# Optimization experiments

Measured on AMD Instinct MI355X. Metric: run time of the kernel, lower is better.

The kernel has to match this reference:

```python
import jax, jax.numpy as jnp
import numpy as np

N_NODES = 50000
N_EDGES = 1600000
IN_DIM = 512
OUT_DIM = 256


def setup_inputs() -> dict:
    key = jax.random.key(0)
    k1, k2, k3, k4, k5, k6 = jax.random.split(key, 6)
    inputs = jax.random.normal(k1, (N_NODES, IN_DIM), dtype=jnp.float32)
    edge_row = jax.random.randint(k2, (N_EDGES,), 0, N_NODES, dtype=jnp.int32)
    edge_col = jax.random.randint(k3, (N_EDGES,), 0, N_NODES, dtype=jnp.int32)
    edge_val = jax.random.uniform(k4, (N_EDGES,), dtype=jnp.float32)
    stdv = 1.0 / np.sqrt(OUT_DIM)
    weight = jax.random.uniform(k5, (IN_DIM, OUT_DIM), dtype=jnp.float32, minval=-stdv, maxval=stdv)
    bias = jax.random.uniform(k6, (OUT_DIM,), dtype=jnp.float32, minval=-stdv, maxval=stdv)
    return {"inputs": inputs, "edge_row": edge_row, "edge_col": edge_col,
            "edge_val": edge_val, "weight": weight, "bias": bias}


def reference(inputs, edge_row, edge_col, edge_val, weight, bias):
    # dense GEMM: [N, in] @ [in, out] -> [N, out]
    support = inputs @ weight
    # SpMM: out[r] += val * support[c] for each edge (r, c, val)
    gathered = edge_val[:, None] * support[edge_col]  # [E, out]
    output = jax.ops.segment_sum(gathered, edge_row, num_segments=N_NODES)
    return output + bias
```

## Files before the change

kernel.cpp:

```cpp
#include <hip/hip_runtime.h>

#define N_NODES 50000
#define N_EDGES 1600000
#define IN_DIM 512
#define OUT_DIM 256

#define BM 128
#define BN 256
#define BK 32
#define APAD 8
#define LDA (BK + APAD)

#define RPB   128
#define NBKT  391
#define CHUNK 4096
#define CAP   5120

typedef unsigned int u32;
typedef unsigned short u16;
typedef short bf16x8 __attribute__((ext_vector_type(8)));
typedef float f32x4 __attribute__((ext_vector_type(4)));

__device__ __forceinline__ float bf_to_f(u16 u) { return __uint_as_float(((u32)u) << 16); }
__device__ __forceinline__ u16 f_to_bf(float f) {
    u32 u = __float_as_uint(f);
    u32 r = (u + 0x7fffu + ((u >> 16) & 1u)) >> 16;
    return (u16)r;
}

__global__ __launch_bounds__(256) void zero_cur(int* __restrict__ cursor) {
    const int i = blockIdx.x * 256 + threadIdx.x;
    if (i < NBKT) cursor[i] = 0;
}

__global__ __launch_bounds__(256) void scatter1(const int* __restrict__ er,
                                                const int* __restrict__ ec,
                                                const float* __restrict__ ev,
                                                int* __restrict__ cursor,
                                                int2* __restrict__ tmp) {
    __shared__ int  hcnt[NBKT];
    __shared__ int  loff[NBKT];
    __shared__ int  gbase[NBKT];
    __shared__ int  sc[512];
    __shared__ int2 estage[CHUNK];
    __shared__ u16  bslot[CHUNK];

    const int t = threadIdx.x;
    const int base = blockIdx.x * CHUNK;
    const int nedge = min(CHUNK, N_EDGES - base);

    for (int k = t; k < NBKT; k += 256) hcnt[k] = 0;
    __syncthreads();

    int w0[16], w1[16], rk[16];
    #pragma unroll
    for (int j = 0; j < 16; ++j) {
        const int i = j * 256 + t;
        rk[j] = -1;
        if (i < nedge) {
            const int e = base + i;
            const int r = er[e];
            const int bk = r >> 7;
            w0[j] = ec[e] | ((r & 127) << 16) | (bk << 23);
            w1[j] = __float_as_int(ev[e]);
            rk[j] = atomicAdd(&hcnt[bk], 1);
        }
    }
    __syncthreads();

    sc[t]       = (t < NBKT) ? hcnt[t] : 0;
    sc[t + 256] = (t + 256 < NBKT) ? hcnt[t + 256] : 0;
    __syncthreads();
    #pragma unroll
    for (int off = 1; off < 512; off <<= 1) {
        const int a0 = (t >= off) ? sc[t - off] : 0;
        const int a1 = sc[t + 256 - off];
        __syncthreads();
        sc[t] += a0;
        sc[t + 256] += a1;
        __syncthreads();
    }
    if (t < NBKT)       loff[t]       = sc[t] - hcnt[t];
    if (t + 256 < NBKT) loff[t + 256] = sc[t + 256] - hcnt[t + 256];

    if (t < NBKT && hcnt[t] > 0)
        gbase[t] = t * CAP + atomicAdd(&cursor[t], hcnt[t]);
    if (t + 256 < NBKT && hcnt[t + 256] > 0)
        gbase[t + 256] = (t + 256) * CAP + atomicAdd(&cursor[t + 256], hcnt[t + 256]);
    __syncthreads();

    #pragma unroll
    for (int j = 0; j < 16; ++j) {
        if (rk[j] >= 0) {
            const int bk = ((u32)w0[j]) >> 23;
            const int s = loff[bk] + rk[j];
            estage[s] = make_int2(w0[j], w1[j]);
            bslot[s]  = (u16)bk;
        }
    }
    __syncthreads();

    for (int s = t; s < nedge; s += 256) {
        const int bk = bslot[s];
        const int2 e2 = estage[s];
        const int gpos = gbase[bk] + (s - loff[bk]);
        if (gpos < (bk + 1) * CAP)
            tmp[gpos] = e2;
    }
}

__global__ __launch_bounds__(256) void bscan(const int* __restrict__ cursor,
                                             int* __restrict__ bucket_base,
                                             int* __restrict__ row_ptr) {
    __shared__ int sc[512];
    __shared__ int orig[512];
    const int t = threadIdx.x;
    const int c0 = (t < NBKT) ? min(cursor[t], CAP) : 0;
    const int c1 = (t + 256 < NBKT) ? min(cursor[t + 256], CAP) : 0;
    sc[t] = c0;       orig[t] = c0;
    sc[t + 256] = c1; orig[t + 256] = c1;
    __syncthreads();
    #pragma unroll
    for (int off = 1; off < 512; off <<= 1) {
        const int a0 = (t >= off) ? sc[t - off] : 0;
        const int a1 = sc[t + 256 - off];
        __syncthreads();
        sc[t] += a0;
        sc[t + 256] += a1;
        __syncthreads();
    }
    if (t < NBKT)       bucket_base[t]       = sc[t] - orig[t];
    if (t + 256 < NBKT) bucket_base[t + 256] = sc[t + 256] - orig[t + 256];
    if (t == 0) row_ptr[N_NODES] = N_EDGES;
}

__global__ __launch_bounds__(256) void scatter2(const int* __restrict__ cursor,
                                                const int* __restrict__ bucket_base,
                                                const int2* __restrict__ tmp,
                                                int* __restrict__ row_ptr,
                                                int2* __restrict__ sedge) {
    __shared__ int rcnt[RPB];
    __shared__ int sc[RPB];
    __shared__ int rcur[RPB];
    const int t = threadIdx.x;
    const int b = blockIdx.x;
    const int n = min(cursor[b], CAP);
    const int2* src = tmp + (size_t)b * CAP;
    const int gb = bucket_base[b];

    if (t < RPB) rcnt[t] = 0;
    __syncthreads();
    for (int i = t; i < n; i += 256)
        atomicAdd(&rcnt[(((u32)src[i].x) >> 16) & 127], 1);
    __syncthreads();

    if (t < RPB) sc[t] = rcnt[t];
    __syncthreads();
    #pragma unroll
    for (int off = 1; off < RPB; off <<= 1) {
        int a = 0;
        if (t < RPB && t >= off) a = sc[t - off];
        __syncthreads();
        if (t < RPB) sc[t] += a;
        __syncthreads();
    }
    if (t < RPB) {
        const int excl = sc[t] - rcnt[t];
        rcur[t] = gb + excl;
        const int row = b * RPB + t;
        if (row < N_NODES) row_ptr[row] = gb + excl;
    }
    __syncthreads();

    for (int i = t; i < n; i += 256) {
        const int2 e2 = src[i];
        const int rloc = (((u32)e2.x) >> 16) & 127;
        const int pos = atomicAdd(&rcur[rloc], 1);
        sedge[pos] = make_int2(e2.x & 0xFFFF, e2.y);
    }
}

__global__ __launch_bounds__(256) void wcvt(const float* __restrict__ W,
                                            u16* __restrict__ WT) {
    const int n  = threadIdx.x;
    const int k0 = blockIdx.x * 4;
    ushort4 o;
    o.x = f_to_bf(W[(size_t)(k0 + 0) * OUT_DIM + n]);
    o.y = f_to_bf(W[(size_t)(k0 + 1) * OUT_DIM + n]);
    o.z = f_to_bf(W[(size_t)(k0 + 2) * OUT_DIM + n]);
    o.w = f_to_bf(W[(size_t)(k0 + 3) * OUT_DIM + n]);
    *(ushort4*)(WT + (size_t)n * IN_DIM + k0) = o;
}

__global__ __launch_bounds__(512) void gemm_mfma(const float* __restrict__ X,
                                                 const u16* __restrict__ WT,
                                                 u16* __restrict__ Sb) {
    __shared__ u16 As[BM * LDA];
    __shared__ u16 Bs[BN * LDA];

    const int tid  = threadIdx.x;
    const int wave = tid >> 6;
    const int lane = tid & 63;
    const int r0   = blockIdx.x * BM;
    const int wm   = (wave & 1) * 64;
    const int wn   = (wave >> 1) * 64;
    const int l15  = lane & 15;
    const int quad = lane >> 4;

    f32x4 acc[4][4];
    #pragma unroll
    for (int i = 0; i < 4; ++i)
        #pragma unroll
        for (int j = 0; j < 4; ++j) acc[i][j] = (f32x4)0.f;

    const int arow = tid >> 2;
    const int akp  = (tid & 3) * 8;
    const int xrow = min(r0 + arow, N_NODES - 1);
    const float* xsrc = X + (size_t)xrow * IN_DIM + akp;
    const int brow = tid >> 1;
    const int bkp  = (tid & 1) * 16;
    const u16* bsrc = WT + (size_t)brow * IN_DIM + bkp;

    for (int kc = 0; kc < IN_DIM; kc += BK) {
        {
            const float4 f0 = *(const float4*)(xsrc + kc + 0);
            const float4 f1 = *(const float4*)(xsrc + kc + 4);
            ushort4 p0, p1;
            p0.x = f_to_bf(f0.x); p0.y = f_to_bf(f0.y); p0.z = f_to_bf(f0.z); p0.w = f_to_bf(f0.w);
            p1.x = f_to_bf(f1.x); p1.y = f_to_bf(f1.y); p1.z = f_to_bf(f1.z); p1.w = f_to_bf(f1.w);
            *(ushort4*)&As[arow * LDA + akp + 0] = p0;
            *(ushort4*)&As[arow * LDA + akp + 4] = p1;
        }
        {
            const uint4 b0 = *(const uint4*)(bsrc + kc);
            const uint4 b1 = *(const uint4*)(bsrc + kc + 8);
            *(uint4*)&Bs[brow * LDA + bkp + 0] = b0;
            *(uint4*)&Bs[brow * LDA + bkp + 8] = b1;
        }
        __syncthreads();

        bf16x8 af[4], bfr[4];
        #pragma unroll
        for (int mt = 0; mt < 4; ++mt)
            af[mt] = *(const bf16x8*)&As[(wm + mt * 16 + l15) * LDA + quad * 8];
        #pragma unroll
        for (int nt = 0; nt < 4; ++nt)
            bfr[nt] = *(const bf16x8*)&Bs[(wn + nt * 16 + l15) * LDA + quad * 8];
        #pragma unroll
        for (int mt = 0; mt < 4; ++mt)
            #pragma unroll
            for (int nt = 0; nt < 4; ++nt)
                acc[mt][nt] = __builtin_amdgcn_mfma_f32_16x16x32_bf16(
                    af[mt], bfr[nt], acc[mt][nt], 0, 0, 0);
        __syncthreads();
    }

    #pragma unroll
    for (int mt = 0; mt < 4; ++mt) {
        #pragma unroll
        for (int r = 0; r < 4; ++r) {
            const int grow = r0 + wm + mt * 16 + quad * 4 + r;
            if (grow < N_NODES) {
                u16* dst = Sb + (size_t)grow * OUT_DIM + wn + l15;
                #pragma unroll
                for (int nt = 0; nt < 4; ++nt)
                    dst[nt * 16] = f_to_bf(acc[mt][nt][r]);
            }
        }
    }
}

__global__ __launch_bounds__(256) void csr_spmm(const int* __restrict__ row_ptr,
                                                const int2* __restrict__ sedge,
                                                const u16* __restrict__ Sb,
                                                const float* __restrict__ bias,
                                                float* __restrict__ out) {
    const int wave = threadIdx.x >> 6;
    const int lane = threadIdx.x & 63;
    const int r = blockIdx.x * 4 + wave;
    if (r >= N_NODES) return;

    const int start = row_ptr[r];
    const int end   = row_ptr[r + 1];

    float4 acc = *(const float4*)(bias + lane * 4);
    const u16* sbase = Sb + lane * 4;
    const long long* se = (const long long*)sedge;

    for (int e = start; e < end; e += 8) {
        int   cols[8];
        float vals[8];
        #pragma unroll
        for (int j = 0; j < 8; ++j) {
            const int idx = min(e + j, end - 1);
            const long long ed = __builtin_nontemporal_load(se + idx);
            cols[j] = (int)(u32)ed;
            vals[j] = (e + j < end) ? __int_as_float((int)(ed >> 32)) : 0.f;
        }

        ushort4 sv[8];
        #pragma unroll
        for (int j = 0; j < 8; ++j)
            sv[j] = *(const ushort4*)(sbase + (size_t)cols[j] * OUT_DIM);

        #pragma unroll
        for (int j = 0; j < 8; ++j) {
            acc.x += vals[j] * bf_to_f(sv[j].x);
            acc.y += vals[j] * bf_to_f(sv[j].y);
            acc.z += vals[j] * bf_to_f(sv[j].z);
            acc.w += vals[j] * bf_to_f(sv[j].w);
        }
    }

    float* dst = out + (size_t)r * OUT_DIM + lane * 4;
    __builtin_nontemporal_store(acc.x, dst + 0);
    __builtin_nontemporal_store(acc.y, dst + 1);
    __builtin_nontemporal_store(acc.z, dst + 2);
    __builtin_nontemporal_store(acc.w, dst + 3);
}

extern "C" void kernel_launch(void* const* d_in, const int* in_sizes, int n_in,
                              void* d_out, int out_size, void* d_ws, size_t ws_size,
                              hipStream_t stream) {
    const float* X    = (const float*)d_in[0];
    const int*   er   = (const int*)d_in[1];
    const int*   ec   = (const int*)d_in[2];
    const float* ev   = (const float*)d_in[3];
    const float* W    = (const float*)d_in[4];
    const float* bias = (const float*)d_in[5];
    float* out        = (float*)d_out;

    char* ws = (char*)d_ws;
    u16*  Sb      = (u16*) (ws);
    int2* tmp     = (int2*)(ws);
    int*  cursor  = (int*) (ws + 16100000);
    int*  bbase   = (int*) (ws + 16110000);
    int2* sedge   = (int2*)(ws + 25600000);
    u16*  WT      = (u16*) (ws + 38400000);
    int*  row_ptr = (int*) (ws + 38662144);

    hipLaunchKernelGGL(zero_cur, dim3(2), dim3(256), 0, stream, cursor);
    hipLaunchKernelGGL(scatter1, dim3((N_EDGES + CHUNK - 1) / CHUNK), dim3(256), 0,
                       stream, er, ec, ev, cursor, tmp);
    hipLaunchKernelGGL(bscan, dim3(1), dim3(256), 0, stream, cursor, bbase, row_ptr);
    hipLaunchKernelGGL(scatter2, dim3(NBKT), dim3(256), 0, stream,
                       cursor, bbase, tmp, row_ptr, sedge);
    hipLaunchKernelGGL(wcvt, dim3(IN_DIM / 4), dim3(256), 0, stream, W, WT);
    hipLaunchKernelGGL(gemm_mfma, dim3((N_NODES + BM - 1) / BM), dim3(512), 0,
                       stream, X, WT, Sb);
    hipLaunchKernelGGL(csr_spmm, dim3((N_NODES + 3) / 4), dim3(256), 0, stream,
                       row_ptr, sedge, Sb, bias, out);
}
```

Before: 376.3 us.

## Fold bucket scan into scatter2, shrink GEMM tile, simplify SpMM edge loads

```diff
diff --git a/kernel.cpp b/kernel.cpp
--- a/kernel.cpp
+++ b/kernel.cpp
@@ -5,7 +5,7 @@
 #define IN_DIM 512
 #define OUT_DIM 256
 
-#define BM 128
+#define BM 64
 #define BN 256
 #define BK 32
 #define APAD 8
@@ -109,12 +109,18 @@
     }
 }
 
-__global__ __launch_bounds__(256) void bscan(const int* __restrict__ cursor,
-                                             int* __restrict__ bucket_base,
-                                             int* __restrict__ row_ptr) {
+__global__ __launch_bounds__(256) void scatter2(const int* __restrict__ cursor,
+                                                const int2* __restrict__ tmp,
+                                                int* __restrict__ row_ptr,
+                                                int2* __restrict__ sedge) {
     __shared__ int sc[512];
     __shared__ int orig[512];
+    __shared__ int rcnt[RPB];
+    __shared__ int rsc[RPB];
+    __shared__ int rcur[RPB];
     const int t = threadIdx.x;
+    const int b = blockIdx.x;
+
     const int c0 = (t < NBKT) ? min(cursor[t], CAP) : 0;
     const int c1 = (t + 256 < NBKT) ? min(cursor[t + 256], CAP) : 0;
     sc[t] = c0;       orig[t] = c0;
@@ -129,24 +135,11 @@
         sc[t + 256] += a1;
         __syncthreads();
     }
-    if (t < NBKT)       bucket_base[t]       = sc[t] - orig[t];
-    if (t + 256 < NBKT) bucket_base[t + 256] = sc[t + 256] - orig[t + 256];
-    if (t == 0) row_ptr[N_NODES] = N_EDGES;
-}
-
-__global__ __launch_bounds__(256) void scatter2(const int* __restrict__ cursor,
-                                                const int* __restrict__ bucket_base,
-                                                const int2* __restrict__ tmp,
-                                                int* __restrict__ row_ptr,
-                                                int2* __restrict__ sedge) {
-    __shared__ int rcnt[RPB];
-    __shared__ int sc[RPB];
-    __shared__ int rcur[RPB];
-    const int t = threadIdx.x;
-    const int b = blockIdx.x;
-    const int n = min(cursor[b], CAP);
+    const int gb = sc[b] - orig[b];
+    const int n  = orig[b];
     const int2* src = tmp + (size_t)b * CAP;
-    const int gb = bucket_base[b];
+
+    if (b == 0 && t == 0) row_ptr[N_NODES] = N_EDGES;
 
     if (t < RPB) rcnt[t] = 0;
     __syncthreads();
@@ -154,18 +147,18 @@
         atomicAdd(&rcnt[(((u32)src[i].x) >> 16) & 127], 1);
     __syncthreads();
 
-    if (t < RPB) sc[t] = rcnt[t];
+    if (t < RPB) rsc[t] = rcnt[t];
     __syncthreads();
     #pragma unroll
     for (int off = 1; off < RPB; off <<= 1) {
         int a = 0;
-        if (t < RPB && t >= off) a = sc[t - off];
-        __syncthreads();
-        if (t < RPB) sc[t] += a;
+        if (t < RPB && t >= off) a = rsc[t - off];
+        __syncthreads();
+        if (t < RPB) rsc[t] += a;
         __syncthreads();
     }
     if (t < RPB) {
-        const int excl = sc[t] - rcnt[t];
+        const int excl = rsc[t] - rcnt[t];
         rcur[t] = gb + excl;
         const int row = b * RPB + t;
         if (row < N_NODES) row_ptr[row] = gb + excl;
@@ -192,7 +185,7 @@
     *(ushort4*)(WT + (size_t)n * IN_DIM + k0) = o;
 }
 
-__global__ __launch_bounds__(512) void gemm_mfma(const float* __restrict__ X,
+__global__ __launch_bounds__(256) void gemm_mfma(const float* __restrict__ X,
                                                  const u16* __restrict__ WT,
                                                  u16* __restrict__ Sb) {
     __shared__ u16 As[BM * LDA];
@@ -202,8 +195,7 @@
     const int wave = tid >> 6;
     const int lane = tid & 63;
     const int r0   = blockIdx.x * BM;
-    const int wm   = (wave & 1) * 64;
-    const int wn   = (wave >> 1) * 64;
+    const int wn   = wave * 64;
     const int l15  = lane & 15;
     const int quad = lane >> 4;
 
@@ -236,13 +228,18 @@
             const uint4 b1 = *(const uint4*)(bsrc + kc + 8);
             *(uint4*)&Bs[brow * LDA + bkp + 0] = b0;
             *(uint4*)&Bs[brow * LDA + bkp + 8] = b1;
+            const u16* bsrc2 = bsrc + (size_t)128 * IN_DIM;
+            const uint4 b2 = *(const uint4*)(bsrc2 + kc);
+            const uint4 b3 = *(const uint4*)(bsrc2 + kc + 8);
+            *(uint4*)&Bs[(brow + 128) * LDA + bkp + 0] = b2;
+            *(uint4*)&Bs[(brow + 128) * LDA + bkp + 8] = b3;
         }
         __syncthreads();
 
         bf16x8 af[4], bfr[4];
         #pragma unroll
         for (int mt = 0; mt < 4; ++mt)
-            af[mt] = *(const bf16x8*)&As[(wm + mt * 16 + l15) * LDA + quad * 8];
+            af[mt] = *(const bf16x8*)&As[(mt * 16 + l15) * LDA + quad * 8];
         #pragma unroll
         for (int nt = 0; nt < 4; ++nt)
             bfr[nt] = *(const bf16x8*)&Bs[(wn + nt * 16 + l15) * LDA + quad * 8];
@@ -259,7 +256,7 @@
     for (int mt = 0; mt < 4; ++mt) {
         #pragma unroll
         for (int r = 0; r < 4; ++r) {
-            const int grow = r0 + wm + mt * 16 + quad * 4 + r;
+            const int grow = r0 + mt * 16 + quad * 4 + r;
             if (grow < N_NODES) {
                 u16* dst = Sb + (size_t)grow * OUT_DIM + wn + l15;
                 #pragma unroll
@@ -285,38 +282,34 @@
 
     float4 acc = *(const float4*)(bias + lane * 4);
     const u16* sbase = Sb + lane * 4;
-    const long long* se = (const long long*)sedge;
 
     for (int e = start; e < end; e += 8) {
-        int   cols[8];
-        float vals[8];
+        int2 ed[8];
         #pragma unroll
         for (int j = 0; j < 8; ++j) {
             const int idx = min(e + j, end - 1);
-            const long long ed = __builtin_nontemporal_load(se + idx);
-            cols[j] = (int)(u32)ed;
-            vals[j] = (e + j < end) ? __int_as_float((int)(ed >> 32)) : 0.f;
-        }
+            ed[j] = sedge[idx];
+        }
+        #pragma unroll
+        for (int j = 0; j < 8; ++j)
+            if (e + j >= end) ed[j].y = 0;
 
         ushort4 sv[8];
         #pragma unroll
         for (int j = 0; j < 8; ++j)
-            sv[j] = *(const ushort4*)(sbase + (size_t)cols[j] * OUT_DIM);
+            sv[j] = *(const ushort4*)(sbase + (size_t)ed[j].x * OUT_DIM);
 
         #pragma unroll
         for (int j = 0; j < 8; ++j) {
-            acc.x += vals[j] * bf_to_f(sv[j].x);
-            acc.y += vals[j] * bf_to_f(sv[j].y);
-            acc.z += vals[j] * bf_to_f(sv[j].z);
-            acc.w += vals[j] * bf_to_f(sv[j].w);
-        }
-    }
-
-    float* dst = out + (size_t)r * OUT_DIM + lane * 4;
-    __builtin_nontemporal_store(acc.x, dst + 0);
-    __builtin_nontemporal_store(acc.y, dst + 1);
-    __builtin_nontemporal_store(acc.z, dst + 2);
-    __builtin_nontemporal_store(acc.w, dst + 3);
+            const float vj = __int_as_float(ed[j].y);
+            acc.x += vj * bf_to_f(sv[j].x);
+            acc.y += vj * bf_to_f(sv[j].y);
+            acc.z += vj * bf_to_f(sv[j].z);
+            acc.w += vj * bf_to_f(sv[j].w);
+        }
+    }
+
+    *(float4*)(out + (size_t)r * OUT_DIM + lane * 4) = acc;
 }
 
 extern "C" void kernel_launch(void* const* d_in, const int* in_sizes, int n_in,
@@ -334,7 +327,6 @@
     u16*  Sb      = (u16*) (ws);
     int2* tmp     = (int2*)(ws);
     int*  cursor  = (int*) (ws + 16100000);
-    int*  bbase   = (int*) (ws + 16110000);
     int2* sedge   = (int2*)(ws + 25600000);
     u16*  WT      = (u16*) (ws + 38400000);
     int*  row_ptr = (int*) (ws + 38662144);
@@ -342,11 +334,10 @@
     hipLaunchKernelGGL(zero_cur, dim3(2), dim3(256), 0, stream, cursor);
     hipLaunchKernelGGL(scatter1, dim3((N_EDGES + CHUNK - 1) / CHUNK), dim3(256), 0,
                        stream, er, ec, ev, cursor, tmp);
-    hipLaunchKernelGGL(bscan, dim3(1), dim3(256), 0, stream, cursor, bbase, row_ptr);
     hipLaunchKernelGGL(scatter2, dim3(NBKT), dim3(256), 0, stream,
-                       cursor, bbase, tmp, row_ptr, sedge);
+                       cursor, tmp, row_ptr, sedge);
     hipLaunchKernelGGL(wcvt, dim3(IN_DIM / 4), dim3(256), 0, stream, W, WT);
-    hipLaunchKernelGGL(gemm_mfma, dim3((N_NODES + BM - 1) / BM), dim3(512), 0,
+    hipLaunchKernelGGL(gemm_mfma, dim3((N_NODES + BM - 1) / BM), dim3(256), 0,
                        stream, X, WT, Sb);
     hipLaunchKernelGGL(csr_spmm, dim3((N_NODES + 3) / 4), dim3(256), 0, stream,
                        row_ptr, sedge, Sb, bias, out);
```

Measured after the change: 358.9 us. 4.6% less time.
